# Performance work log

Hardware: AMD Instinct MI355X
Metric: run time of the kernel (lower is better)

## Reference

```python
import jax, jax.numpy as jnp
import numpy as np

B, T, MAX_ITEMS = 128, 50, 32
NUM_PRODUCT, E, EW = 100000, 128, 16
D = E + EW  # rnn input/hidden size


def setup_inputs() -> dict:
    key = jax.random.key(0)
    ks = jax.random.split(key, 10)
    # items: 0 is padding; keep roughly half the slots padded (ragged baskets)
    items = jax.random.randint(ks[0], (B, T, MAX_ITEMS), 1, NUM_PRODUCT)
    keep = jax.random.uniform(ks[1], (B, T, MAX_ITEMS)) < 0.5
    keep = keep.at[:, :, 0].set(True)  # at least one item per basket
    items = jnp.where(keep, items, 0)
    flag = jax.random.randint(ks[2], (B, T, 1), 0, 2)
    x = jnp.concatenate([items, flag], axis=-1)  # [B,T,MAX_ITEMS+1], last col = flag
    lengths = jnp.full((B,), T, dtype=jnp.int64)
    hidden = jnp.zeros((1, B, D), dtype=jnp.float32)
    s_e = 1.0 / np.sqrt(E)
    s_d = 1.0 / np.sqrt(D)
    encode_w = jax.random.uniform(ks[3], (NUM_PRODUCT, E), minval=-0.1, maxval=0.1)
    encode_w = encode_w.at[0].set(0.0)  # padding_idx=0
    wchange_w = jax.random.normal(ks[4], (2, EW)) * 0.1
    wchange_w = wchange_w.at[0].set(0.0)  # padding_idx=0
    w_ih = jax.random.uniform(ks[5], (3 * D, D), minval=-s_d, maxval=s_d)
    w_hh = jax.random.uniform(ks[6], (3 * D, D), minval=-s_d, maxval=s_d)
    b_ih = jax.random.uniform(ks[7], (3 * D,), minval=-s_d, maxval=s_d)
    b_hh = jax.random.uniform(ks[8], (3 * D,), minval=-s_d, maxval=s_d)
    fc_w = jax.random.uniform(ks[9], (E, D), minval=-s_d, maxval=s_d)
    fc_b = jnp.zeros((E,), dtype=jnp.float32)
    return {"x": x, "lengths": lengths, "hidden": hidden,
            "encode_w": encode_w, "wchange_w": wchange_w,
            "w_ih": w_ih, "w_hh": w_hh, "b_ih": b_ih, "b_hh": b_hh,
            "fc_w": fc_w, "fc_b": fc_b}


def _embed_baskets(x, encode_w, wchange_w):
    items = x[..., :-1]                      # [B,T,I] product ids, 0 = pad
    flag = x[..., -1]                        # [B,T] 0/1 weight-change flag
    emb = encode_w[items]                    # [B,T,I,E] fused ragged gather
    mask = (items != 0).astype(emb.dtype)[..., None]
    cnt = jnp.maximum(mask.sum(axis=2), 1.0)
    pooled = (emb * mask).sum(axis=2) / cnt  # avg pool over real items [B,T,E]
    w = wchange_w[flag]                      # [B,T,EW]
    return jnp.concatenate([pooled, w], axis=-1)  # [B,T,D]


def _gru(seq, h0, w_ih, w_hh, b_ih, b_hh):
    # seq: [B,T,D], h0: [B,D]; torch GRU cell math
    def step(h, x_t):
        gi = x_t @ w_ih.T + b_ih             # [B,3D]
        gh = h @ w_hh.T + b_hh
        i_r, i_z, i_n = jnp.split(gi, 3, axis=-1)
        h_r, h_z, h_n = jnp.split(gh, 3, axis=-1)
        r = jax.nn.sigmoid(i_r + h_r)
        z = jax.nn.sigmoid(i_z + h_z)
        n = jnp.tanh(i_n + r * h_n)
        h_new = (1.0 - z) * n + z * h
        return h_new, h_new
    h_last, outs = jax.lax.scan(step, h0, jnp.swapaxes(seq, 0, 1))
    return jnp.swapaxes(outs, 0, 1), h_last  # [B,T,D], [B,D]


def reference(x, lengths, hidden, encode_w, wchange_w, w_ih, w_hh, b_ih, b_hh, fc_w, fc_b):
    seq = _embed_baskets(x, encode_w, wchange_w)         # [B,T,D]
    out, h_last = _gru(seq, hidden[0], w_ih, w_hh, b_ih, b_hh)
    dynamic_user = out @ fc_w.T + fc_b                   # [B,T,E]
    return dynamic_user, h_last[None]                    # h_u: [1,B,D]
```

## Files before the change

kernel.cpp:

```cpp
#include <hip/hip_runtime.h>
#include <math.h>

#define B_   128
#define T_   50
#define MI_  32
#define E_   128
#define EW_  16
#define D_   144
#define G_   432
#define N_   (B_*T_)

__global__ __launch_bounds__(256) void embed_kernel(
    const int* __restrict__ x,
    const float* __restrict__ encode_w,
    const float* __restrict__ wchange_w,
    float* __restrict__ seq)
{
    int n = blockIdx.x;
    int tid = threadIdx.x;
    int i = tid >> 3;
    int j = tid & 7;

    __shared__ int xi[33];
    __shared__ __align__(16) float part[32 * 132];
    __shared__ float cntf[32];

    if (tid < 33) xi[tid] = x[n * 33 + tid];
    __syncthreads();

    int it = xi[i];
    const float* row = &encode_w[(size_t)it * E_];
    float4 v0 = *(const float4*)&row[16 * j + 0];
    float4 v1 = *(const float4*)&row[16 * j + 4];
    float4 v2 = *(const float4*)&row[16 * j + 8];
    float4 v3 = *(const float4*)&row[16 * j + 12];

    float* p = &part[i * 132 + 16 * j];
    *(float4*)&p[0]  = v0;
    *(float4*)&p[4]  = v1;
    *(float4*)&p[8]  = v2;
    *(float4*)&p[12] = v3;
    if (j == 0) cntf[i] = (it != 0) ? 1.f : 0.f;
    __syncthreads();

    if (tid < E_) {
        int c = tid;
        float s = 0.f, cn = 0.f;
        #pragma unroll
        for (int k = 0; k < 32; ++k) {
            s  += part[k * 132 + c];
            cn += cntf[k];
        }
        seq[n * D_ + c] = s / fmaxf(cn, 1.f);
    } else if (tid < E_ + EW_) {
        int c = tid - E_;
        seq[n * D_ + E_ + c] = wchange_w[xi[32] * EW_ + c];
    }
}

#define GK   144
#define GBK  48
#define GPAD 68

__global__ __launch_bounds__(256) void gemm_bias_kernel(
    const float* __restrict__ A,
    const float* __restrict__ Bw,
    const float* __restrict__ bias,
    float* __restrict__ C,
    int M, int N)
{
    __shared__ float As[GBK * GPAD];
    __shared__ float Bs[GBK * GPAD];

    int tid = threadIdx.x;
    int row0 = blockIdx.x * 64;
    int col0 = blockIdx.y * 64;
    int tx = tid & 15;
    int ty = tid >> 4;

    float acc[4][4] = {};

    int sr = tid >> 2;
    int skq0 = tid & 3;

    for (int k0 = 0; k0 < GK; k0 += GBK) {
        __syncthreads();
        #pragma unroll
        for (int i = 0; i < 3; ++i) {
            int kq = skq0 + i * 4;
            float4 a = *(const float4*)&A[(size_t)(row0 + sr) * GK + k0 + kq * 4];
            int nrow = col0 + sr;
            float4 b = make_float4(0.f, 0.f, 0.f, 0.f);
            if (nrow < N)
                b = *(const float4*)&Bw[(size_t)nrow * GK + k0 + kq * 4];
            As[(kq * 4 + 0) * GPAD + sr] = a.x;
            As[(kq * 4 + 1) * GPAD + sr] = a.y;
            As[(kq * 4 + 2) * GPAD + sr] = a.z;
            As[(kq * 4 + 3) * GPAD + sr] = a.w;
            Bs[(kq * 4 + 0) * GPAD + sr] = b.x;
            Bs[(kq * 4 + 1) * GPAD + sr] = b.y;
            Bs[(kq * 4 + 2) * GPAD + sr] = b.z;
            Bs[(kq * 4 + 3) * GPAD + sr] = b.w;
        }
        __syncthreads();

        #pragma unroll 4
        for (int k = 0; k < GBK; ++k) {
            float4 a4 = *(const float4*)&As[k * GPAD + ty * 4];
            float4 b4 = *(const float4*)&Bs[k * GPAD + tx * 4];
            float av[4] = {a4.x, a4.y, a4.z, a4.w};
            float bv[4] = {b4.x, b4.y, b4.z, b4.w};
            #pragma unroll
            for (int i = 0; i < 4; ++i)
                #pragma unroll
                for (int j = 0; j < 4; ++j)
                    acc[i][j] = fmaf(av[i], bv[j], acc[i][j]);
        }
    }

    int c = col0 + tx * 4;
    if (c < N) {
        float4 bb = *(const float4*)&bias[c];
        #pragma unroll
        for (int i = 0; i < 4; ++i) {
            int r = row0 + ty * 4 + i;
            float4 o;
            o.x = acc[i][0] + bb.x;
            o.y = acc[i][1] + bb.y;
            o.z = acc[i][2] + bb.z;
            o.w = acc[i][3] + bb.w;
            *(float4*)&C[(size_t)r * N + c] = o;
        }
    }
}

template<int CTRL>
__device__ __forceinline__ float dpp_xor_add(float x) {
    int y = __builtin_amdgcn_mov_dpp(__float_as_int(x), CTRL, 0xF, 0xF, true);
    return x + __int_as_float(y);
}

__global__ __launch_bounds__(576) void gru_kernel(
    const float* __restrict__ gi,
    const float* __restrict__ w_hh,
    const float* __restrict__ b_hh,
    const float* __restrict__ h0,
    float* __restrict__ hseq,
    float* __restrict__ hlast)
{
    int b = blockIdx.x;
    int tid = threadIdx.x;
    int g = tid >> 3;
    int s = tid & 7;
    int k0 = s * 20;

    __shared__ __align__(16) float h[160];
    __shared__ float gh[G_];

    float w[6][20];
    #pragma unroll
    for (int r = 0; r < 6; ++r) {
        const float* wrow = &w_hh[(size_t)(6 * g + r) * D_];
        #pragma unroll
        for (int q = 0; q < 5; ++q) {
            int k = k0 + 4 * q;
            float4 t = make_float4(0.f, 0.f, 0.f, 0.f);
            if (k < D_) t = *(const float4*)&wrow[k];
            w[r][4 * q + 0] = t.x;
            w[r][4 * q + 1] = t.y;
            w[r][4 * q + 2] = t.z;
            w[r][4 * q + 3] = t.w;
        }
    }
    float bias = (s < 6) ? b_hh[6 * g + s] : 0.f;

    if (tid < 160) h[tid] = (tid < D_) ? h0[b * D_ + tid] : 0.f;
    __syncthreads();

    float gir = 0.f, giz = 0.f, gin = 0.f;
    if (tid < D_) {
        const float* gp = &gi[(size_t)(b * T_) * G_];
        gir = gp[tid];
        giz = gp[D_ + tid];
        gin = gp[2 * D_ + tid];
    }

    for (int t = 0; t < T_; ++t) {
        int n = b * T_ + t;

        float girU = gir, gizU = giz, ginU = gin;
        if (tid < D_ && t + 1 < T_) {
            const float* gp = &gi[(size_t)(n + 1) * G_];
            gir = gp[tid];
            giz = gp[D_ + tid];
            gin = gp[2 * D_ + tid];
        }

        float hv[20];
        #pragma unroll
        for (int q = 0; q < 5; ++q) {
            float4 t4 = *(const float4*)&h[k0 + 4 * q];
            hv[4 * q + 0] = t4.x;
            hv[4 * q + 1] = t4.y;
            hv[4 * q + 2] = t4.z;
            hv[4 * q + 3] = t4.w;
        }

        float a0 = 0.f, a1 = 0.f, a2 = 0.f, a3 = 0.f, a4 = 0.f, a5 = 0.f;
        #pragma unroll
        for (int kk = 0; kk < 20; ++kk) {
            float hk = hv[kk];
            a0 = fmaf(w[0][kk], hk, a0);
            a1 = fmaf(w[1][kk], hk, a1);
            a2 = fmaf(w[2][kk], hk, a2);
            a3 = fmaf(w[3][kk], hk, a3);
            a4 = fmaf(w[4][kk], hk, a4);
            a5 = fmaf(w[5][kk], hk, a5);
        }

        a0 = dpp_xor_add<0xB1>(a0); a0 = dpp_xor_add<0x4E>(a0); a0 = dpp_xor_add<0x141>(a0);
        a1 = dpp_xor_add<0xB1>(a1); a1 = dpp_xor_add<0x4E>(a1); a1 = dpp_xor_add<0x141>(a1);
        a2 = dpp_xor_add<0xB1>(a2); a2 = dpp_xor_add<0x4E>(a2); a2 = dpp_xor_add<0x141>(a2);
        a3 = dpp_xor_add<0xB1>(a3); a3 = dpp_xor_add<0x4E>(a3); a3 = dpp_xor_add<0x141>(a3);
        a4 = dpp_xor_add<0xB1>(a4); a4 = dpp_xor_add<0x4E>(a4); a4 = dpp_xor_add<0x141>(a4);
        a5 = dpp_xor_add<0xB1>(a5); a5 = dpp_xor_add<0x4E>(a5); a5 = dpp_xor_add<0x141>(a5);

        float myacc = a0;
        if (s == 1) myacc = a1;
        if (s == 2) myacc = a2;
        if (s == 3) myacc = a3;
        if (s == 4) myacc = a4;
        if (s == 5) myacc = a5;
        if (s < 6) gh[6 * g + s] = myacc + bias;
        __syncthreads();

        if (tid < D_) {
            float r = 1.f / (1.f + __expf(-(girU + gh[tid])));
            float z = 1.f / (1.f + __expf(-(gizU + gh[D_ + tid])));
            float narg = ginU + r * gh[2 * D_ + tid];
            narg = fminf(fmaxf(narg, -15.f), 15.f);
            float e2 = __expf(-2.f * narg);
            float nn = (1.f - e2) / (1.f + e2);
            float hn = (1.f - z) * nn + z * h[tid];
            hseq[(size_t)n * D_ + tid] = hn;
            h[tid] = hn;
        }
        __syncthreads();
    }

    if (tid < D_) hlast[b * D_ + tid] = h[tid];
}

extern "C" void kernel_launch(void* const* d_in, const int* in_sizes, int n_in,
                              void* d_out, int out_size, void* d_ws, size_t ws_size,
                              hipStream_t stream)
{
    const int*   x         = (const int*)d_in[0];
    const float* hidden    = (const float*)d_in[2];
    const float* encode_w  = (const float*)d_in[3];
    const float* wchange_w = (const float*)d_in[4];
    const float* w_ih      = (const float*)d_in[5];
    const float* w_hh      = (const float*)d_in[6];
    const float* b_ih      = (const float*)d_in[7];
    const float* b_hh      = (const float*)d_in[8];
    const float* fc_w      = (const float*)d_in[9];
    const float* fc_b      = (const float*)d_in[10];

    float* out = (float*)d_out;
    float* ws  = (float*)d_ws;
    float* seq  = ws;
    float* gi   = ws + 921600;
    float* hseq = ws + 921600 + 2764800;

    embed_kernel<<<N_, 256, 0, stream>>>(x, encode_w, wchange_w, seq);

    gemm_bias_kernel<<<dim3(N_ / 64, (G_ + 63) / 64), 256, 0, stream>>>(
        seq, w_ih, b_ih, gi, N_, G_);

    gru_kernel<<<B_, 576, 0, stream>>>(gi, w_hh, b_hh, hidden, hseq,
                                       out + (size_t)N_ * E_);

    gemm_bias_kernel<<<dim3(N_ / 64, E_ / 64), 256, 0, stream>>>(
        hseq, fc_w, fc_b, out, N_, E_);
}
```

Baseline: 187.0 us.

## Replace tiled input and output GEMMs with register-resident weight matvec kernels

Both dense projections (input-to-gates and the final fc layer) drop the shared-memory tiled GEMM. They now use kernels where each thread keeps a slice of the weight matrix in registers, stages 25 rows of activations in shared memory, and reduces partial dot products across 8 lanes with DPP. This avoids reloading weight tiles per output tile and reuses the GRU-style layout. The cost is fewer, larger blocks (256) with heavy register use and narrow, strided stores.

New measurement: 193.5 us. 3.4% more time.

```diff
diff --git a/kernel.cpp b/kernel.cpp
--- a/kernel.cpp
+++ b/kernel.cpp
@@ -58,109 +58,45 @@
     }
 }
 
-#define GK   144
-#define GBK  48
-#define GPAD 68
-
-__global__ __launch_bounds__(256) void gemm_bias_kernel(
-    const float* __restrict__ A,
-    const float* __restrict__ Bw,
-    const float* __restrict__ bias,
-    float* __restrict__ C,
-    int M, int N)
-{
-    __shared__ float As[GBK * GPAD];
-    __shared__ float Bs[GBK * GPAD];
-
-    int tid = threadIdx.x;
-    int row0 = blockIdx.x * 64;
-    int col0 = blockIdx.y * 64;
-    int tx = tid & 15;
-    int ty = tid >> 4;
-
-    float acc[4][4] = {};
-
-    int sr = tid >> 2;
-    int skq0 = tid & 3;
-
-    for (int k0 = 0; k0 < GK; k0 += GBK) {
-        __syncthreads();
-        #pragma unroll
-        for (int i = 0; i < 3; ++i) {
-            int kq = skq0 + i * 4;
-            float4 a = *(const float4*)&A[(size_t)(row0 + sr) * GK + k0 + kq * 4];
-            int nrow = col0 + sr;
-            float4 b = make_float4(0.f, 0.f, 0.f, 0.f);
-            if (nrow < N)
-                b = *(const float4*)&Bw[(size_t)nrow * GK + k0 + kq * 4];
-            As[(kq * 4 + 0) * GPAD + sr] = a.x;
-            As[(kq * 4 + 1) * GPAD + sr] = a.y;
-            As[(kq * 4 + 2) * GPAD + sr] = a.z;
-            As[(kq * 4 + 3) * GPAD + sr] = a.w;
-            Bs[(kq * 4 + 0) * GPAD + sr] = b.x;
-            Bs[(kq * 4 + 1) * GPAD + sr] = b.y;
-            Bs[(kq * 4 + 2) * GPAD + sr] = b.z;
-            Bs[(kq * 4 + 3) * GPAD + sr] = b.w;
-        }
-        __syncthreads();
-
-        #pragma unroll 4
-        for (int k = 0; k < GBK; ++k) {
-            float4 a4 = *(const float4*)&As[k * GPAD + ty * 4];
-            float4 b4 = *(const float4*)&Bs[k * GPAD + tx * 4];
-            float av[4] = {a4.x, a4.y, a4.z, a4.w};
-            float bv[4] = {b4.x, b4.y, b4.z, b4.w};
-            #pragma unroll
-            for (int i = 0; i < 4; ++i)
-                #pragma unroll
-                for (int j = 0; j < 4; ++j)
-                    acc[i][j] = fmaf(av[i], bv[j], acc[i][j]);
-        }
-    }
-
-    int c = col0 + tx * 4;
-    if (c < N) {
-        float4 bb = *(const float4*)&bias[c];
-        #pragma unroll
-        for (int i = 0; i < 4; ++i) {
-            int r = row0 + ty * 4 + i;
-            float4 o;
-            o.x = acc[i][0] + bb.x;
-            o.y = acc[i][1] + bb.y;
-            o.z = acc[i][2] + bb.z;
-            o.w = acc[i][3] + bb.w;
-            *(float4*)&C[(size_t)r * N + c] = o;
-        }
-    }
-}
-
 template<int CTRL>
 __device__ __forceinline__ float dpp_xor_add(float x) {
     int y = __builtin_amdgcn_mov_dpp(__float_as_int(x), CTRL, 0xF, 0xF, true);
     return x + __int_as_float(y);
 }
-
-__global__ __launch_bounds__(576) void gru_kernel(
-    const float* __restrict__ gi,
-    const float* __restrict__ w_hh,
-    const float* __restrict__ b_hh,
-    const float* __restrict__ h0,
-    float* __restrict__ hseq,
-    float* __restrict__ hlast)
-{
-    int b = blockIdx.x;
+#define DPP_RED3(v) \
+    v = dpp_xor_add<0xB1>(v); v = dpp_xor_add<0x4E>(v); v = dpp_xor_add<0x141>(v);
+
+__global__ __launch_bounds__(576) void gi_matvec_kernel(
+    const float* __restrict__ seq,
+    const float* __restrict__ w_ih,
+    const float* __restrict__ b_ih,
+    float* __restrict__ gi)
+{
+    int n0 = blockIdx.x * 25;
     int tid = threadIdx.x;
     int g = tid >> 3;
     int s = tid & 7;
     int k0 = s * 20;
 
-    __shared__ __align__(16) float h[160];
-    __shared__ float gh[G_];
+    __shared__ __align__(16) float sq[25 * 160];
+
+    {
+        float4* d4 = (float4*)sq;
+        const float4* s4 = (const float4*)(seq + (size_t)n0 * D_);
+        for (int idx = tid; idx < 100; idx += 576) {
+            int i = idx >> 2, p = idx & 3;
+            d4[i * 40 + 36 + p] = make_float4(0.f, 0.f, 0.f, 0.f);
+        }
+        for (int idx = tid; idx < 900; idx += 576) {
+            int i = idx / 36, q = idx - i * 36;
+            d4[i * 40 + q] = s4[i * 36 + q];
+        }
+    }
 
     float w[6][20];
     #pragma unroll
     for (int r = 0; r < 6; ++r) {
-        const float* wrow = &w_hh[(size_t)(6 * g + r) * D_];
+        const float* wrow = &w_ih[(size_t)(6 * g + r) * D_];
         #pragma unroll
         for (int q = 0; q < 5; ++q) {
             int k = k0 + 4 * q;
@@ -172,40 +108,21 @@
             w[r][4 * q + 3] = t.w;
         }
     }
-    float bias = (s < 6) ? b_hh[6 * g + s] : 0.f;
-
-    if (tid < 160) h[tid] = (tid < D_) ? h0[b * D_ + tid] : 0.f;
-    __syncthreads();
-
-    float gir = 0.f, giz = 0.f, gin = 0.f;
-    if (tid < D_) {
-        const float* gp = &gi[(size_t)(b * T_) * G_];
-        gir = gp[tid];
-        giz = gp[D_ + tid];
-        gin = gp[2 * D_ + tid];
-    }
-
-    for (int t = 0; t < T_; ++t) {
-        int n = b * T_ + t;
-
-        float girU = gir, gizU = giz, ginU = gin;
-        if (tid < D_ && t + 1 < T_) {
-            const float* gp = &gi[(size_t)(n + 1) * G_];
-            gir = gp[tid];
-            giz = gp[D_ + tid];
-            gin = gp[2 * D_ + tid];
-        }
-
+    float bias = (s < 6) ? b_ih[6 * g + s] : 0.f;
+    __syncthreads();
+
+    const float* hp = sq + k0;
+    float* gp = gi + (size_t)n0 * G_ + 6 * g + s;
+    for (int i = 0; i < 25; ++i) {
         float hv[20];
         #pragma unroll
         for (int q = 0; q < 5; ++q) {
-            float4 t4 = *(const float4*)&h[k0 + 4 * q];
+            float4 t4 = *(const float4*)&hp[i * 160 + 4 * q];
             hv[4 * q + 0] = t4.x;
             hv[4 * q + 1] = t4.y;
             hv[4 * q + 2] = t4.z;
             hv[4 * q + 3] = t4.w;
         }
-
         float a0 = 0.f, a1 = 0.f, a2 = 0.f, a3 = 0.f, a4 = 0.f, a5 = 0.f;
         #pragma unroll
         for (int kk = 0; kk < 20; ++kk) {
@@ -217,13 +134,168 @@
             a4 = fmaf(w[4][kk], hk, a4);
             a5 = fmaf(w[5][kk], hk, a5);
         }
-
-        a0 = dpp_xor_add<0xB1>(a0); a0 = dpp_xor_add<0x4E>(a0); a0 = dpp_xor_add<0x141>(a0);
-        a1 = dpp_xor_add<0xB1>(a1); a1 = dpp_xor_add<0x4E>(a1); a1 = dpp_xor_add<0x141>(a1);
-        a2 = dpp_xor_add<0xB1>(a2); a2 = dpp_xor_add<0x4E>(a2); a2 = dpp_xor_add<0x141>(a2);
-        a3 = dpp_xor_add<0xB1>(a3); a3 = dpp_xor_add<0x4E>(a3); a3 = dpp_xor_add<0x141>(a3);
-        a4 = dpp_xor_add<0xB1>(a4); a4 = dpp_xor_add<0x4E>(a4); a4 = dpp_xor_add<0x141>(a4);
-        a5 = dpp_xor_add<0xB1>(a5); a5 = dpp_xor_add<0x4E>(a5); a5 = dpp_xor_add<0x141>(a5);
+        DPP_RED3(a0); DPP_RED3(a1); DPP_RED3(a2);
+        DPP_RED3(a3); DPP_RED3(a4); DPP_RED3(a5);
+        float myacc = a0;
+        if (s == 1) myacc = a1;
+        if (s == 2) myacc = a2;
+        if (s == 3) myacc = a3;
+        if (s == 4) myacc = a4;
+        if (s == 5) myacc = a5;
+        if (s < 6) gp[(size_t)i * G_] = myacc + bias;
+    }
+}
+
+__global__ __launch_bounds__(512) void fc_matvec_kernel(
+    const float* __restrict__ hseq,
+    const float* __restrict__ fc_w,
+    const float* __restrict__ fc_b,
+    float* __restrict__ dyn)
+{
+    int n0 = blockIdx.x * 25;
+    int tid = threadIdx.x;
+    int g = tid >> 3;
+    int s = tid & 7;
+    int k0 = s * 20;
+
+    __shared__ __align__(16) float sq[25 * 160];
+
+    {
+        float4* d4 = (float4*)sq;
+        const float4* s4 = (const float4*)(hseq + (size_t)n0 * D_);
+        for (int idx = tid; idx < 100; idx += 512) {
+            int i = idx >> 2, p = idx & 3;
+            d4[i * 40 + 36 + p] = make_float4(0.f, 0.f, 0.f, 0.f);
+        }
+        for (int idx = tid; idx < 900; idx += 512) {
+            int i = idx / 36, q = idx - i * 36;
+            d4[i * 40 + q] = s4[i * 36 + q];
+        }
+    }
+
+    float w[2][20];
+    #pragma unroll
+    for (int r = 0; r < 2; ++r) {
+        const float* wrow = &fc_w[(size_t)(2 * g + r) * D_];
+        #pragma unroll
+        for (int q = 0; q < 5; ++q) {
+            int k = k0 + 4 * q;
+            float4 t = make_float4(0.f, 0.f, 0.f, 0.f);
+            if (k < D_) t = *(const float4*)&wrow[k];
+            w[r][4 * q + 0] = t.x;
+            w[r][4 * q + 1] = t.y;
+            w[r][4 * q + 2] = t.z;
+            w[r][4 * q + 3] = t.w;
+        }
+    }
+    float bias = (s < 2) ? fc_b[2 * g + s] : 0.f;
+    __syncthreads();
+
+    const float* hp = sq + k0;
+    float* gp = dyn + (size_t)n0 * E_ + 2 * g + s;
+    for (int i = 0; i < 25; ++i) {
+        float hv[20];
+        #pragma unroll
+        for (int q = 0; q < 5; ++q) {
+            float4 t4 = *(const float4*)&hp[i * 160 + 4 * q];
+            hv[4 * q + 0] = t4.x;
+            hv[4 * q + 1] = t4.y;
+            hv[4 * q + 2] = t4.z;
+            hv[4 * q + 3] = t4.w;
+        }
+        float f0 = 0.f, f1 = 0.f;
+        #pragma unroll
+        for (int kk = 0; kk < 20; ++kk) {
+            float hk = hv[kk];
+            f0 = fmaf(w[0][kk], hk, f0);
+            f1 = fmaf(w[1][kk], hk, f1);
+        }
+        DPP_RED3(f0); DPP_RED3(f1);
+        float myacc = (s == 0) ? f0 : f1;
+        if (s < 2) gp[(size_t)i * E_] = myacc + bias;
+    }
+}
+
+__global__ __launch_bounds__(576) void gru_kernel(
+    const float* __restrict__ gi,
+    const float* __restrict__ w_hh,
+    const float* __restrict__ b_hh,
+    const float* __restrict__ h0,
+    float* __restrict__ hseq,
+    float* __restrict__ hlast)
+{
+    int b = blockIdx.x;
+    int tid = threadIdx.x;
+    int g = tid >> 3;
+    int s = tid & 7;
+    int k0 = s * 20;
+
+    __shared__ __align__(16) float h[160];
+    __shared__ float gh[G_];
+
+    float w[6][20];
+    #pragma unroll
+    for (int r = 0; r < 6; ++r) {
+        const float* wrow = &w_hh[(size_t)(6 * g + r) * D_];
+        #pragma unroll
+        for (int q = 0; q < 5; ++q) {
+            int k = k0 + 4 * q;
+            float4 t = make_float4(0.f, 0.f, 0.f, 0.f);
+            if (k < D_) t = *(const float4*)&wrow[k];
+            w[r][4 * q + 0] = t.x;
+            w[r][4 * q + 1] = t.y;
+            w[r][4 * q + 2] = t.z;
+            w[r][4 * q + 3] = t.w;
+        }
+    }
+    float bias = (s < 6) ? b_hh[6 * g + s] : 0.f;
+
+    if (tid < 160) h[tid] = (tid < D_) ? h0[b * D_ + tid] : 0.f;
+    __syncthreads();
+
+    float gir = 0.f, giz = 0.f, gin = 0.f;
+    if (tid < D_) {
+        const float* gp = &gi[(size_t)(b * T_) * G_];
+        gir = gp[tid];
+        giz = gp[D_ + tid];
+        gin = gp[2 * D_ + tid];
+    }
+
+    for (int t = 0; t < T_; ++t) {
+        int n = b * T_ + t;
+
+        float girU = gir, gizU = giz, ginU = gin;
+        if (tid < D_ && t + 1 < T_) {
+            const float* gp = &gi[(size_t)(n + 1) * G_];
+            gir = gp[tid];
+            giz = gp[D_ + tid];
+            gin = gp[2 * D_ + tid];
+        }
+
+        float hv[20];
+        #pragma unroll
+        for (int q = 0; q < 5; ++q) {
+            float4 t4 = *(const float4*)&h[k0 + 4 * q];
+            hv[4 * q + 0] = t4.x;
+            hv[4 * q + 1] = t4.y;
+            hv[4 * q + 2] = t4.z;
+            hv[4 * q + 3] = t4.w;
+        }
+
+        float a0 = 0.f, a1 = 0.f, a2 = 0.f, a3 = 0.f, a4 = 0.f, a5 = 0.f;
+        #pragma unroll
+        for (int kk = 0; kk < 20; ++kk) {
+            float hk = hv[kk];
+            a0 = fmaf(w[0][kk], hk, a0);
+            a1 = fmaf(w[1][kk], hk, a1);
+            a2 = fmaf(w[2][kk], hk, a2);
+            a3 = fmaf(w[3][kk], hk, a3);
+            a4 = fmaf(w[4][kk], hk, a4);
+            a5 = fmaf(w[5][kk], hk, a5);
+        }
+
+        DPP_RED3(a0); DPP_RED3(a1); DPP_RED3(a2);
+        DPP_RED3(a3); DPP_RED3(a4); DPP_RED3(a5);
 
         float myacc = a0;
         if (s == 1) myacc = a1;
@@ -274,12 +346,10 @@
 
     embed_kernel<<<N_, 256, 0, stream>>>(x, encode_w, wchange_w, seq);
 
-    gemm_bias_kernel<<<dim3(N_ / 64, (G_ + 63) / 64), 256, 0, stream>>>(
-        seq, w_ih, b_ih, gi, N_, G_);
+    gi_matvec_kernel<<<256, 576, 0, stream>>>(seq, w_ih, b_ih, gi);
 
     gru_kernel<<<B_, 576, 0, stream>>>(gi, w_hh, b_hh, hidden, hseq,
                                        out + (size_t)N_ * E_);
 
-    gemm_bias_kernel<<<dim3(N_ / 64, E_ / 64), 256, 0, stream>>>(
-        hseq, fc_w, fc_b, out, N_, E_);
-}
+    fc_matvec_kernel<<<256, 512, 0, stream>>>(hseq, fc_w, fc_b, out);
+}
```
